# Performance work log

Hardware: AMD Instinct MI355X
Metric: run time of the kernel (lower is better)

The kernel has to match this reference:

```python
import jax, jax.numpy as jnp
import numpy as np

N_NODES = 50000
N_EDGES = 800000
D_IN, H1, H2, N_CLASSES = 128, 128, 64, 2


def setup_inputs() -> dict:
    key = jax.random.key(0)
    ks = jax.random.split(key, 8)
    x = jax.random.normal(ks[0], (N_NODES, D_IN), dtype=jnp.float32)
    edge_index = jax.random.randint(ks[1], (2, N_EDGES), 0, N_NODES, dtype=jnp.int64)
    s = 1.0 / np.sqrt(D_IN)
    W1 = jax.random.uniform(ks[2], (D_IN, H1), jnp.float32, -s, s)
    b1 = jnp.zeros((H1,), jnp.float32)
    s = 1.0 / np.sqrt(H1)
    W2 = jax.random.uniform(ks[3], (H1, H2), jnp.float32, -s, s)
    b2 = jnp.zeros((H2,), jnp.float32)
    s = 1.0 / np.sqrt(H2)
    Wo = jax.random.uniform(ks[4], (H2, N_CLASSES), jnp.float32, -s, s)
    bo = jax.random.uniform(ks[5], (N_CLASSES,), jnp.float32, -s, s)
    return {"x": x, "edge_index": edge_index, "W1": W1, "b1": b1,
            "W2": W2, "b2": b2, "Wo": Wo, "bo": bo}


def _gcn_conv(x, W, b, src, dst, n_nodes):
    # PyG GCNConv: add self loops, symmetric normalization deg^{-1/2} A deg^{-1/2}
    h = x @ W  # [N, out]
    ones = jnp.ones((src.shape[0],), h.dtype)
    deg = jax.ops.segment_sum(ones, dst, num_segments=n_nodes) + 1.0  # +1 self loop
    dinv = jax.lax.rsqrt(deg)  # deg >= 1 always (self loops)
    coef = dinv[src] * dinv[dst]  # [E]
    msg = h[src] * coef[:, None]  # [E, out] gather
    agg = jax.ops.segment_sum(msg, dst, num_segments=n_nodes)  # scatter-add
    agg = agg + h * (dinv * dinv)[:, None]  # self-loop contribution
    return agg + b


def reference(x, edge_index, W1, b1, W2, b2, Wo, bo):
    src, dst = edge_index[0], edge_index[1]
    n = x.shape[0]
    h = jax.nn.relu(_gcn_conv(x, W1, b1, src, dst, n))
    # dropout p=0.25 is identity in eval mode
    h = jax.nn.relu(_gcn_conv(h, W2, b2, src, dst, n))
    logits = h @ Wo + bo
    return jax.nn.log_softmax(logits, axis=1)
```

## Files before the change

### kernel.cpp

```cpp
#include <hip/hip_runtime.h>
#include <stdint.h>

#define N_NODES 50000
#define N_EDGES 800000
#define CAP 80
#define ZROW N_NODES

typedef __attribute__((ext_vector_type(8))) short short8;
typedef __attribute__((ext_vector_type(4))) float floatx4;

__device__ __forceinline__ float bflo(uint32_t u) { return __uint_as_float(u << 16); }
__device__ __forceinline__ float bfhi(uint32_t u) { return __uint_as_float(u & 0xffff0000u); }
__device__ __forceinline__ unsigned short f2b(float f) {
    uint32_t u = __float_as_uint(f);
    u += 0x7fffu + ((u >> 16) & 1u);
    return (unsigned short)(u >> 16);
}

__global__ void k_prep(const float* __restrict__ W1, const float* __restrict__ W2,
                       unsigned short* __restrict__ Wt1, unsigned short* __restrict__ Wt2,
                       int* __restrict__ counts) {
    int gid = blockIdx.x * 256 + threadIdx.x;
    if (gid < 16384) {
        int k = gid >> 7, n = gid & 127;
        Wt1[n * 128 + k] = f2b(W1[gid]);
    } else if (gid < 24576) {
        int j = gid - 16384;
        int k = j >> 6, n = j & 63;
        Wt2[n * 128 + k] = f2b(W2[j]);
    } else if (gid < 24576 + N_NODES) {
        counts[gid - 24576] = 0;
    }
}

__global__ __launch_bounds__(256) void k_scat(const int* __restrict__ src,
                                              const int* __restrict__ dst,
                                              int* __restrict__ counts,
                                              int* __restrict__ csr) {
    int i = blockIdx.x * 256 + threadIdx.x;
    if (i >= N_EDGES / 8) return;
    const int4* s4 = (const int4*)(src + i * 8);
    const int4* d4 = (const int4*)(dst + i * 8);
    int4 sa = s4[0], sb = s4[1];
    int4 da = d4[0], db = d4[1];
    int r0 = atomicAdd(&counts[da.x], 1);
    int r1 = atomicAdd(&counts[da.y], 1);
    int r2 = atomicAdd(&counts[da.z], 1);
    int r3 = atomicAdd(&counts[da.w], 1);
    int r4 = atomicAdd(&counts[db.x], 1);
    int r5 = atomicAdd(&counts[db.y], 1);
    int r6 = atomicAdd(&counts[db.z], 1);
    int r7 = atomicAdd(&counts[db.w], 1);
    if (r0 < CAP) csr[da.x * CAP + r0] = sa.x;
    if (r1 < CAP) csr[da.y * CAP + r1] = sa.y;
    if (r2 < CAP) csr[da.z * CAP + r2] = sa.z;
    if (r3 < CAP) csr[da.w * CAP + r3] = sa.w;
    if (r4 < CAP) csr[db.x * CAP + r4] = sb.x;
    if (r5 < CAP) csr[db.y * CAP + r5] = sb.y;
    if (r6 < CAP) csr[db.z * CAP + r6] = sb.z;
    if (r7 < CAP) csr[db.w * CAP + r7] = sb.w;
}

__global__ __launch_bounds__(256) void k_gemm1(const float* __restrict__ x,
                                               const unsigned short* __restrict__ Wt1,
                                               const int* __restrict__ counts,
                                               unsigned short* __restrict__ h1s,
                                               unsigned short* __restrict__ h2s) {
    __shared__ unsigned short At[64 * 136];
    __shared__ unsigned short Bt[128 * 136];
    int t = threadIdx.x;
    int row0 = blockIdx.x * 64;
    for (int i = t; i < 2048; i += 256) {
        int n = i >> 4, kc = (i & 15) * 8;
        *(uint4*)&Bt[n * 136 + kc] = *(const uint4*)(Wt1 + n * 128 + kc);
    }
    for (int i = t; i < 1024; i += 256) {
        int r = i >> 4, kc = (i & 15) * 8;
        int g = row0 + r; if (g >= N_NODES) g = N_NODES - 1;
        const float* p = x + g * 128 + kc;
        float4 a = *(const float4*)p, b = *(const float4*)(p + 4);
        uint4 o;
        o.x = (uint32_t)f2b(a.x) | ((uint32_t)f2b(a.y) << 16);
        o.y = (uint32_t)f2b(a.z) | ((uint32_t)f2b(a.w) << 16);
        o.z = (uint32_t)f2b(b.x) | ((uint32_t)f2b(b.y) << 16);
        o.w = (uint32_t)f2b(b.z) | ((uint32_t)f2b(b.w) << 16);
        *(uint4*)&At[r * 136 + kc] = o;
    }
    __syncthreads();
    int wv = t >> 6, lane = t & 63;
    int m = lane & 15, qd = lane >> 4;
    floatx4 acc[8];
    #pragma unroll
    for (int c = 0; c < 8; c++) acc[c] = (floatx4){0.f, 0.f, 0.f, 0.f};
    const unsigned short* ap = &At[(wv * 16 + m) * 136 + qd * 8];
    const unsigned short* bp = &Bt[m * 136 + qd * 8];
    #pragma unroll
    for (int kk = 0; kk < 4; kk++) {
        short8 af = *(const short8*)(ap + kk * 32);
        #pragma unroll
        for (int c = 0; c < 8; c++) {
            short8 bf = *(const short8*)(bp + c * 16 * 136 + kk * 32);
            acc[c] = __builtin_amdgcn_mfma_f32_16x16x32_bf16(af, bf, acc[c], 0, 0, 0);
        }
    }
    #pragma unroll
    for (int reg = 0; reg < 4; reg++) {
        int g = row0 + wv * 16 + qd * 4 + reg;
        if (g < N_NODES) {
            float di = rsqrtf((float)counts[g] + 1.0f);
            #pragma unroll
            for (int c = 0; c < 8; c++)
                h1s[g * 128 + c * 16 + m] = f2b(di * acc[c][reg]);
        } else {
            #pragma unroll
            for (int c = 0; c < 8; c++)
                h1s[g * 128 + c * 16 + m] = 0;
            #pragma unroll
            for (int c = 0; c < 4; c++)
                h2s[g * 64 + c * 16 + m] = 0;
        }
    }
}

__global__ __launch_bounds__(256) void k_agg1g2(const unsigned short* __restrict__ h1s,
                                                const unsigned short* __restrict__ Wt2,
                                                const int* __restrict__ csr,
                                                const int* __restrict__ counts,
                                                const float* __restrict__ b1,
                                                unsigned short* __restrict__ h2s) {
    __shared__ unsigned short Bt[64 * 136];
    __shared__ unsigned short At[16 * 136];
    int t = threadIdx.x;
    for (int i = t; i < 1024; i += 256) {
        int n = i >> 4, kc = (i & 15) * 8;
        *(uint4*)&Bt[n * 136 + kc] = *(const uint4*)(Wt2 + n * 128 + kc);
    }
    int wv = t >> 6, lane = t & 63;
    int q = lane >> 4, l = lane & 15;
    int v0 = blockIdx.x * 16;
    int v = v0 + wv * 4 + q;
    int n = counts[v];
    float dv = rsqrtf((float)n + 1.0f);
    int n_eff = min(n, CAP);
    const int* cs = csr + v * CAP;
    int nmax = n_eff;
    nmax = max(nmax, __shfl_xor(nmax, 16));
    nmax = max(nmax, __shfl_xor(nmax, 32));
    float a0, a1, a2, a3, a4, a5, a6, a7;
    {
        uint4 p = *(const uint4*)(h1s + v * 128 + l * 8);
        a0 = bflo(p.x); a1 = bfhi(p.x); a2 = bflo(p.y); a3 = bfhi(p.y);
        a4 = bflo(p.z); a5 = bfhi(p.z); a6 = bflo(p.w); a7 = bfhi(p.w);
    }
    for (int base = 0; base < nmax; base += 16) {
        int idx = base + l;
        int e = (idx < n_eff) ? cs[idx] : ZROW;
        int mm = nmax - base; if (mm > 16) mm = 16;
        #pragma unroll 4
        for (int i = 0; i < mm; i++) {
            int s = __shfl(e, (q << 4) + i);
            uint4 p = *(const uint4*)(h1s + s * 128 + l * 8);
            a0 += bflo(p.x); a1 += bfhi(p.x); a2 += bflo(p.y); a3 += bfhi(p.y);
            a4 += bflo(p.z); a5 += bfhi(p.z); a6 += bflo(p.w); a7 += bfhi(p.w);
        }
    }
    {
        float4 bL = *(const float4*)(b1 + l * 8);
        float4 bH = *(const float4*)(b1 + l * 8 + 4);
        a0 = fmaxf(fmaf(dv, a0, bL.x), 0.f); a1 = fmaxf(fmaf(dv, a1, bL.y), 0.f);
        a2 = fmaxf(fmaf(dv, a2, bL.z), 0.f); a3 = fmaxf(fmaf(dv, a3, bL.w), 0.f);
        a4 = fmaxf(fmaf(dv, a4, bH.x), 0.f); a5 = fmaxf(fmaf(dv, a5, bH.y), 0.f);
        a6 = fmaxf(fmaf(dv, a6, bH.z), 0.f); a7 = fmaxf(fmaf(dv, a7, bH.w), 0.f);
        uint4 o;
        o.x = (uint32_t)f2b(a0) | ((uint32_t)f2b(a1) << 16);
        o.y = (uint32_t)f2b(a2) | ((uint32_t)f2b(a3) << 16);
        o.z = (uint32_t)f2b(a4) | ((uint32_t)f2b(a5) << 16);
        o.w = (uint32_t)f2b(a6) | ((uint32_t)f2b(a7) << 16);
        *(uint4*)&At[(wv * 4 + q) * 136 + l * 8] = o;
    }
    __syncthreads();
    int m = lane & 15, qd = lane >> 4;
    floatx4 acc = (floatx4){0.f, 0.f, 0.f, 0.f};
    const unsigned short* ap = &At[m * 136 + qd * 8];
    const unsigned short* bp = &Bt[(wv * 16 + m) * 136 + qd * 8];
    #pragma unroll
    for (int kk = 0; kk < 4; kk++) {
        short8 af = *(const short8*)(ap + kk * 32);
        short8 bf = *(const short8*)(bp + kk * 32);
        acc = __builtin_amdgcn_mfma_f32_16x16x32_bf16(af, bf, acc, 0, 0, 0);
    }
    #pragma unroll
    for (int reg = 0; reg < 4; reg++) {
        int g = v0 + qd * 4 + reg;
        float dg = rsqrtf((float)counts[g] + 1.0f);
        h2s[g * 64 + wv * 16 + m] = f2b(dg * acc[reg]);
    }
}

__global__ __launch_bounds__(256) void k_agg2(const unsigned short* __restrict__ h2s,
                                              const int* __restrict__ csr,
                                              const int* __restrict__ counts,
                                              const float* __restrict__ b2,
                                              const float* __restrict__ Wo,
                                              const float* __restrict__ bo,
                                              float* __restrict__ out) {
    int wave = (blockIdx.x * 256 + threadIdx.x) >> 6;
    int lane = threadIdx.x & 63;
    int q = lane >> 4, l = lane & 15;
    int v = wave * 4 + q;
    int n = counts[v];
    float dv = rsqrtf((float)n + 1.0f);
    int n_eff = min(n, CAP);
    const int* cs = csr + v * CAP;
    int nmax = n_eff;
    nmax = max(nmax, __shfl_xor(nmax, 16));
    nmax = max(nmax, __shfl_xor(nmax, 32));
    float a0, a1, a2, a3;
    {
        uint2 p = *(const uint2*)(h2s + v * 64 + l * 4);
        a0 = bflo(p.x); a1 = bfhi(p.x); a2 = bflo(p.y); a3 = bfhi(p.y);
    }
    for (int base = 0; base < nmax; base += 16) {
        int idx = base + l;
        int e = (idx < n_eff) ? cs[idx] : ZROW;
        int mm = nmax - base; if (mm > 16) mm = 16;
        #pragma unroll 4
        for (int i = 0; i < mm; i++) {
            int s = __shfl(e, (q << 4) + i);
            uint2 p = *(const uint2*)(h2s + s * 64 + l * 4);
            a0 += bflo(p.x); a1 += bfhi(p.x); a2 += bflo(p.y); a3 += bfhi(p.y);
        }
    }
    float4 bb = *(const float4*)(b2 + l * 4);
    a0 = fmaxf(fmaf(dv, a0, bb.x), 0.f);
    a1 = fmaxf(fmaf(dv, a1, bb.y), 0.f);
    a2 = fmaxf(fmaf(dv, a2, bb.z), 0.f);
    a3 = fmaxf(fmaf(dv, a3, bb.w), 0.f);
    float4 w01 = *(const float4*)(Wo + l * 8);
    float4 w23 = *(const float4*)(Wo + l * 8 + 4);
    float l0 = a0 * w01.x + a1 * w01.z + a2 * w23.x + a3 * w23.z;
    float l1 = a0 * w01.y + a1 * w01.w + a2 * w23.y + a3 * w23.w;
    #pragma unroll
    for (int off = 8; off > 0; off >>= 1) {
        l0 += __shfl_xor(l0, off);
        l1 += __shfl_xor(l1, off);
    }
    if (l == 0) {
        float2 bof = *(const float2*)bo;
        l0 += bof.x; l1 += bof.y;
        float m = fmaxf(l0, l1);
        float ls = m + __logf(__expf(l0 - m) + __expf(l1 - m));
        *(float2*)(out + v * 2) = make_float2(l0 - ls, l1 - ls);
    }
}

extern "C" void kernel_launch(void* const* d_in, const int* in_sizes, int n_in,
                              void* d_out, int out_size, void* d_ws, size_t ws_size,
                              hipStream_t stream) {
    const float* x  = (const float*)d_in[0];
    const int* ei   = (const int*)d_in[1];
    const float* W1 = (const float*)d_in[2];
    const float* b1 = (const float*)d_in[3];
    const float* W2 = (const float*)d_in[4];
    const float* b2 = (const float*)d_in[5];
    const float* Wo = (const float*)d_in[6];
    const float* bo = (const float*)d_in[7];
    float* out      = (float*)d_out;
    const int* src = ei;
    const int* dst = ei + N_EDGES;

    char* w = (char*)d_ws;
    int* counts = (int*)(w + 0);
    int* csr    = (int*)(w + 200704);
    unsigned short* Wt1 = (unsigned short*)(w + 16200704);
    unsigned short* Wt2 = (unsigned short*)(w + 16233472);
    unsigned short* h1s = (unsigned short*)(w + 16249856);
    unsigned short* h2s = (unsigned short*)(w + 29062144);

    k_prep  <<<292, 256, 0, stream>>>(W1, W2, Wt1, Wt2, counts);
    k_scat  <<<391, 256, 0, stream>>>(src, dst, counts, csr);
    k_gemm1 <<<782, 256, 0, stream>>>(x, Wt1, counts, h1s, h2s);
    k_agg1g2<<<3125, 256, 0, stream>>>(h1s, Wt2, csr, counts, b1, h2s);
    k_agg2  <<<3125, 256, 0, stream>>>(h2s, csr, counts, b2, Wo, bo, out);
}
```

Measured before the change: 192.9 us.

## Fold weight prep into scatter kernel, memset counts, and double agg1g2 block size

Removes the separate k_prep launch. Counts are now zeroed with hipMemsetAsync, and the weight transpose/bf16 conversion runs in extra blocks appended to the k_scat grid. The fused agg1g2 kernel now handles 32 nodes per 512-thread block, so each Wt2 load into LDS is amortized over twice as many rows, with a 2x4 wave tiling for the MFMA. Bounds checks are added for the partial last block. The cost is larger blocks, which may lower occupancy, and a memset call that may have its own launch cost.

```diff
diff --git a/kernel.cpp b/kernel.cpp
--- a/kernel.cpp
+++ b/kernel.cpp
@@ -17,27 +17,28 @@
     return (unsigned short)(u >> 16);
 }
 
-__global__ void k_prep(const float* __restrict__ W1, const float* __restrict__ W2,
-                       unsigned short* __restrict__ Wt1, unsigned short* __restrict__ Wt2,
-                       int* __restrict__ counts) {
-    int gid = blockIdx.x * 256 + threadIdx.x;
-    if (gid < 16384) {
-        int k = gid >> 7, n = gid & 127;
-        Wt1[n * 128 + k] = f2b(W1[gid]);
-    } else if (gid < 24576) {
-        int j = gid - 16384;
-        int k = j >> 6, n = j & 63;
-        Wt2[n * 128 + k] = f2b(W2[j]);
-    } else if (gid < 24576 + N_NODES) {
-        counts[gid - 24576] = 0;
-    }
-}
-
 __global__ __launch_bounds__(256) void k_scat(const int* __restrict__ src,
                                               const int* __restrict__ dst,
                                               int* __restrict__ counts,
-                                              int* __restrict__ csr) {
-    int i = blockIdx.x * 256 + threadIdx.x;
+                                              int* __restrict__ csr,
+                                              const float* __restrict__ W1,
+                                              const float* __restrict__ W2,
+                                              unsigned short* __restrict__ Wt1,
+                                              unsigned short* __restrict__ Wt2) {
+    int b = blockIdx.x;
+    if (b >= 391) {
+        int gid = (b - 391) * 256 + threadIdx.x;
+        if (gid < 16384) {
+            int k = gid >> 7, n = gid & 127;
+            Wt1[n * 128 + k] = f2b(W1[gid]);
+        } else {
+            int j = gid - 16384;
+            int k = j >> 6, n = j & 63;
+            Wt2[n * 128 + k] = f2b(W2[j]);
+        }
+        return;
+    }
+    int i = b * 256 + threadIdx.x;
     if (i >= N_EDGES / 8) return;
     const int4* s4 = (const int4*)(src + i * 8);
     const int4* d4 = (const int4*)(dst + i * 8);
@@ -122,24 +123,26 @@
     }
 }
 
-__global__ __launch_bounds__(256) void k_agg1g2(const unsigned short* __restrict__ h1s,
+__global__ __launch_bounds__(512) void k_agg1g2(const unsigned short* __restrict__ h1s,
                                                 const unsigned short* __restrict__ Wt2,
                                                 const int* __restrict__ csr,
                                                 const int* __restrict__ counts,
                                                 const float* __restrict__ b1,
                                                 unsigned short* __restrict__ h2s) {
     __shared__ unsigned short Bt[64 * 136];
-    __shared__ unsigned short At[16 * 136];
+    __shared__ unsigned short At[32 * 136];
     int t = threadIdx.x;
-    for (int i = t; i < 1024; i += 256) {
+    for (int i = t; i < 1024; i += 512) {
         int n = i >> 4, kc = (i & 15) * 8;
         *(uint4*)&Bt[n * 136 + kc] = *(const uint4*)(Wt2 + n * 128 + kc);
     }
     int wv = t >> 6, lane = t & 63;
     int q = lane >> 4, l = lane & 15;
-    int v0 = blockIdx.x * 16;
+    int v0 = blockIdx.x * 32;
     int v = v0 + wv * 4 + q;
-    int n = counts[v];
+    int vloc = wv * 4 + q;
+    bool valid = v < N_NODES;
+    int n = valid ? counts[v] : 0;
     float dv = rsqrtf((float)n + 1.0f);
     int n_eff = min(n, CAP);
     const int* cs = csr + v * CAP;
@@ -148,7 +151,8 @@
     nmax = max(nmax, __shfl_xor(nmax, 32));
     float a0, a1, a2, a3, a4, a5, a6, a7;
     {
-        uint4 p = *(const uint4*)(h1s + v * 128 + l * 8);
+        int vr = valid ? v : ZROW;
+        uint4 p = *(const uint4*)(h1s + vr * 128 + l * 8);
         a0 = bflo(p.x); a1 = bfhi(p.x); a2 = bflo(p.y); a3 = bfhi(p.y);
         a4 = bflo(p.z); a5 = bfhi(p.z); a6 = bflo(p.w); a7 = bfhi(p.w);
     }
@@ -176,13 +180,14 @@
         o.y = (uint32_t)f2b(a2) | ((uint32_t)f2b(a3) << 16);
         o.z = (uint32_t)f2b(a4) | ((uint32_t)f2b(a5) << 16);
         o.w = (uint32_t)f2b(a6) | ((uint32_t)f2b(a7) << 16);
-        *(uint4*)&At[(wv * 4 + q) * 136 + l * 8] = o;
+        *(uint4*)&At[vloc * 136 + l * 8] = o;
     }
     __syncthreads();
+    int rt = wv >> 2, ct = wv & 3;
     int m = lane & 15, qd = lane >> 4;
     floatx4 acc = (floatx4){0.f, 0.f, 0.f, 0.f};
-    const unsigned short* ap = &At[m * 136 + qd * 8];
-    const unsigned short* bp = &Bt[(wv * 16 + m) * 136 + qd * 8];
+    const unsigned short* ap = &At[(rt * 16 + m) * 136 + qd * 8];
+    const unsigned short* bp = &Bt[(ct * 16 + m) * 136 + qd * 8];
     #pragma unroll
     for (int kk = 0; kk < 4; kk++) {
         short8 af = *(const short8*)(ap + kk * 32);
@@ -191,9 +196,11 @@
     }
     #pragma unroll
     for (int reg = 0; reg < 4; reg++) {
-        int g = v0 + qd * 4 + reg;
-        float dg = rsqrtf((float)counts[g] + 1.0f);
-        h2s[g * 64 + wv * 16 + m] = f2b(dg * acc[reg]);
+        int g = v0 + rt * 16 + qd * 4 + reg;
+        if (g < N_NODES) {
+            float dg = rsqrtf((float)counts[g] + 1.0f);
+            h2s[g * 64 + ct * 16 + m] = f2b(dg * acc[reg]);
+        }
     }
 }
 
@@ -277,9 +284,9 @@
     unsigned short* h1s = (unsigned short*)(w + 16249856);
     unsigned short* h2s = (unsigned short*)(w + 29062144);
 
-    k_prep  <<<292, 256, 0, stream>>>(W1, W2, Wt1, Wt2, counts);
-    k_scat  <<<391, 256, 0, stream>>>(src, dst, counts, csr);
+    hipMemsetAsync(counts, 0, N_NODES * sizeof(int), stream);
+    k_scat  <<<487, 256, 0, stream>>>(src, dst, counts, csr, W1, W2, Wt1, Wt2);
     k_gemm1 <<<782, 256, 0, stream>>>(x, Wt1, counts, h1s, h2s);
-    k_agg1g2<<<3125, 256, 0, stream>>>(h1s, Wt2, csr, counts, b1, h2s);
+    k_agg1g2<<<1563, 512, 0, stream>>>(h1s, Wt2, csr, counts, b1, h2s);
     k_agg2  <<<3125, 256, 0, stream>>>(h2s, csr, counts, b2, Wo, bo, out);
 }
```

Measured after the change: 194.0 us. Within noise of the previous version (+0.6%).
